# Performance work log

Measured on AMD Instinct MI355X. Metric: run time of the kernel, lower is better.

## Reference

```python
import jax, jax.numpy as jnp
import numpy as np

N = 50000
E = 800000
D = 128
L = 2
EPS = 1e-12  # BatchNorm1d eps in the module
NEG_SLOPE = 0.2  # PyG GATConv default leaky_relu slope


def setup_inputs() -> dict:
    key = jax.random.key(0)
    ks = jax.random.split(key, 12)
    x = jax.random.normal(ks[0], (N, D), dtype=jnp.float32)
    # edges guaranteed non-self (GATConv removes then re-adds self loops)
    src = jax.random.randint(ks[1], (E,), 0, N)
    off = jax.random.randint(ks[2], (E,), 1, N)
    dst = (src + off) % N
    edge_index = jnp.stack([src, dst]).astype(jnp.int64)
    scale = 1.0 / np.sqrt(D)
    Ws = jax.random.normal(ks[3], (L, D, D), dtype=jnp.float32) * scale
    a_src = jax.random.normal(ks[4], (L, D), dtype=jnp.float32) * scale
    a_dst = jax.random.normal(ks[5], (L, D), dtype=jnp.float32) * scale
    bias = jax.random.normal(ks[6], (L, D), dtype=jnp.float32) * 0.01
    gamma = jnp.ones((L, D), dtype=jnp.float32)
    beta = jnp.zeros((L, D), dtype=jnp.float32)
    run_mean = jax.random.normal(ks[7], (L, D), dtype=jnp.float32) * 0.01
    run_var = jax.random.uniform(ks[8], (L, D), minval=0.5, maxval=1.5, dtype=jnp.float32)
    return {"x": x, "edge_index": edge_index, "Ws": Ws, "a_src": a_src,
            "a_dst": a_dst, "bias": bias, "gamma": gamma, "beta": beta,
            "run_mean": run_mean, "run_var": run_var}


def _gat_layer(x, src, dst, W, asrc, adst, b):
    # x: [N, d_in]; W: [d_in, D]
    h = x @ W  # [N, D]
    e = jnp.take(h @ asrc, src) + jnp.take(h @ adst, dst)  # [E'] per-edge score
    e = jnp.where(e > 0, e, NEG_SLOPE * e)  # leaky_relu
    # segment softmax over destination node
    m = jax.ops.segment_max(e, dst, num_segments=N)
    ee = jnp.exp(e - jnp.take(m, dst))
    s = jax.ops.segment_sum(ee, dst, num_segments=N)
    alpha = ee / jnp.take(s, dst)
    # scatter-aggregate weighted source features
    msg = alpha[:, None] * jnp.take(h, src, axis=0)  # [E', D]
    out = jax.ops.segment_sum(msg, dst, num_segments=N)
    return out + b


def reference(x, edge_index, Ws, a_src, a_dst, bias, gamma, beta, run_mean, run_var):
    src, dst = edge_index[0], edge_index[1]
    # GATConv add_self_loops=True
    loops = jnp.arange(N, dtype=src.dtype)
    src = jnp.concatenate([src, loops])
    dst = jnp.concatenate([dst, loops])
    for i in range(L):
        x = _gat_layer(x, src, dst, Ws[i], a_src[i], a_dst[i], bias[i])
        # BatchNorm1d (eval mode, running stats) + ReLU
        x = (x - run_mean[i]) * (gamma[i] * jax.lax.rsqrt(run_var[i] + EPS)) + beta[i]
        x = jax.nn.relu(x)
    return x
```

## Files before the change

### kernel.cpp

```cpp
#include <hip/hip_runtime.h>

constexpr int Dd = 128;
constexpr float BN_EPS = 1e-12f;
constexpr float NEG_SLOPE = 0.2f;

using bf16x8 = __attribute__((ext_vector_type(8))) short;
using f32x4  = __attribute__((ext_vector_type(4))) float;

__device__ __forceinline__ ushort f2bf(float f) {
    unsigned u = __float_as_uint(f);
    return (ushort)((u + 0x7fffu + ((u >> 16) & 1u)) >> 16);
}

__global__ __launch_bounds__(256) void wprep_zero_kernel(
    const float* __restrict__ W, ushort* __restrict__ Wt, int* __restrict__ cntc)
{
    int t = threadIdx.x;
    if (blockIdx.x >= 2) {
        cntc[t] = 0;
        return;
    }
    __shared__ float lds[32][33];
    const float* Wl = W + (size_t)blockIdx.x * Dd * Dd;
    ushort* Wo = Wt + (size_t)blockIdx.x * Dd * Dd;
    int r = t >> 3, c4 = (t & 7) << 2;
    for (int tk = 0; tk < 4; ++tk)
    for (int tn = 0; tn < 4; ++tn) {
        int k0 = tk * 32, n0 = tn * 32;
        float4 v = *(const float4*)&Wl[(size_t)(k0 + r) * Dd + n0 + c4];
        lds[r][c4] = v.x; lds[r][c4 + 1] = v.y; lds[r][c4 + 2] = v.z; lds[r][c4 + 3] = v.w;
        __syncthreads();
        ushort4 o;
        o.x = f2bf(lds[c4 + 0][r]); o.y = f2bf(lds[c4 + 1][r]);
        o.z = f2bf(lds[c4 + 2][r]); o.w = f2bf(lds[c4 + 3][r]);
        *(ushort4*)&Wo[(size_t)(n0 + r) * Dd + k0 + c4] = o;
        __syncthreads();
    }
}

__global__ __launch_bounds__(256) void coarse_hist_kernel(
    const int* __restrict__ dst, int* __restrict__ cntc, int E, int NB)
{
    __shared__ int lh[256];
    int t = threadIdx.x;
    lh[t] = 0;
    __syncthreads();
    for (int e = blockIdx.x * 256 + t; e < E; e += gridDim.x * 256)
        atomicAdd(&lh[dst[e] >> 8], 1);
    __syncthreads();
    if (t < NB && lh[t]) atomicAdd(&cntc[t], lh[t]);
}

__global__ __launch_bounds__(256) void coarse_scan_kernel(
    const int* __restrict__ cntc, int* __restrict__ base,
    int* __restrict__ cursor, int NB, int E)
{
    __shared__ int lds[256];
    int t = threadIdx.x;
    int v0 = (t < NB) ? cntc[t] : 0;
    lds[t] = v0;
    __syncthreads();
    for (int o = 1; o < 256; o <<= 1) {
        int v = (t >= o) ? lds[t - o] : 0;
        __syncthreads();
        lds[t] += v;
        __syncthreads();
    }
    int excl = lds[t] - v0;
    if (t < NB) { base[t] = excl; cursor[t] = excl; }
    if (t == 0) base[NB] = E;
}

__global__ __launch_bounds__(256) void partition_kernel(
    const int* __restrict__ src, const int* __restrict__ dst,
    int* __restrict__ cursor, unsigned* __restrict__ gpart, int E)
{
    __shared__ int h[256], lb[256], gs[256], cur[256];
    __shared__ unsigned staged[4096];
    const int t = threadIdx.x;
    const int c0 = blockIdx.x * 4096;
    const int count = min(4096, E - c0);

    h[t] = 0; cur[t] = 0;
    __syncthreads();
#pragma unroll
    for (int j = 0; j < 16; ++j) {
        int idx = j * 256 + t;
        if (idx < count) atomicAdd(&h[dst[c0 + idx] >> 8], 1);
    }
    __syncthreads();
    {
        int v0 = h[t];
        lb[t] = v0;
        __syncthreads();
        for (int o = 1; o < 256; o <<= 1) {
            int v = (t >= o) ? lb[t - o] : 0;
            __syncthreads();
            lb[t] += v;
            __syncthreads();
        }
        lb[t] -= v0;
    }
    if (h[t]) gs[t] = atomicAdd(&cursor[t], h[t]);
    __syncthreads();
#pragma unroll
    for (int j = 0; j < 16; ++j) {
        int idx = j * 256 + t;
        if (idx < count) {
            int d = dst[c0 + idx], s = src[c0 + idx];
            int b = d >> 8;
            int pos = lb[b] + atomicAdd(&cur[b], 1);
            staged[pos] = (unsigned)s | ((unsigned)(d & 255) << 16) | ((unsigned)b << 24);
        }
    }
    __syncthreads();
#pragma unroll
    for (int j = 0; j < 16; ++j) {
        int idx = j * 256 + t;
        if (idx < count) {
            unsigned p = staged[idx];
            int b = p >> 24;
            gpart[gs[b] + (idx - lb[b])] = p;
        }
    }
}

__global__ __launch_bounds__(256) void bucket_csr_kernel(
    const unsigned* __restrict__ gpart, const int* __restrict__ base,
    int* __restrict__ rowptr, int* __restrict__ ssrc, int N, int NB, int E)
{
    __shared__ int h[256], lb[256], cur[256];
    const int t = threadIdx.x;
    const int b = blockIdx.x;
    const int cb = base[b], ce = base[b + 1];
    const int cnt = ce - cb;

    h[t] = 0; cur[t] = 0;
    __syncthreads();
    for (int o = t; o < cnt; o += 256)
        atomicAdd(&h[(gpart[cb + o] >> 16) & 255], 1);
    __syncthreads();
    {
        int v0 = h[t];
        lb[t] = v0;
        __syncthreads();
        for (int o = 1; o < 256; o <<= 1) {
            int v = (t >= o) ? lb[t - o] : 0;
            __syncthreads();
            lb[t] += v;
            __syncthreads();
        }
        lb[t] -= v0;
    }
    int n0 = b * 256 + t;
    if (n0 < N) rowptr[n0] = cb + lb[t];
    if (b == 0 && t == 0) rowptr[N] = E;
    __syncthreads();
    for (int o = t; o < cnt; o += 256) {
        unsigned p = gpart[cb + o];
        int n = (p >> 16) & 255;
        int pos = lb[n] + atomicAdd(&cur[n], 1);
        ssrc[cb + pos] = (int)(p & 0xFFFFu);
    }
}

template<bool BF16IN>
__global__ __launch_bounds__(256) void gemm_mfma(
    const void* __restrict__ Xv, const ushort* __restrict__ Wt,
    const float* __restrict__ asrc, const float* __restrict__ adst,
    ushort* __restrict__ Hb, float* __restrict__ hs, float* __restrict__ hd, int N)
{
    __shared__ ushort Xs[64 * 128];
    __shared__ ushort Bs[128 * 128];

    const int t = threadIdx.x;
    const int lane = t & 63, wid = t >> 6;
    const int row0 = blockIdx.x * 64;

    if constexpr (BF16IN) {
        const ushort* X = (const ushort*)Xv;
#pragma unroll
        for (int p = 0; p < 4; ++p) {
            int id = t + p * 256;
            int r = id >> 4, b16 = id & 15;
            int g = row0 + r;
            uint4 v = make_uint4(0, 0, 0, 0);
            if (g < N) v = *(const uint4*)&X[(size_t)g * Dd + b16 * 8];
            *(uint4*)&Xs[r * 128 + ((b16 ^ (r & 15)) << 3)] = v;
        }
    } else {
        const float* X = (const float*)Xv;
#pragma unroll
        for (int p = 0; p < 8; ++p) {
            int id = t + p * 256;
            int r = id >> 5, c4g = id & 31;
            int g = row0 + r;
            float4 v = make_float4(0.f, 0.f, 0.f, 0.f);
            if (g < N) v = *(const float4*)&X[(size_t)g * Dd + c4g * 4];
            ushort4 o; o.x = f2bf(v.x); o.y = f2bf(v.y); o.z = f2bf(v.z); o.w = f2bf(v.w);
            int b16 = c4g >> 1, sub = c4g & 1;
            *(ushort4*)&Xs[r * 128 + (((b16 ^ (r & 15)) << 3) | (sub << 2))] = o;
        }
    }
#pragma unroll
    for (int p = 0; p < 8; ++p) {
        int id = t + p * 256;
        int n = id >> 4, b16 = id & 15;
        uint4 v = *(const uint4*)&Wt[(size_t)n * 128 + b16 * 8];
        *(uint4*)&Bs[n * 128 + ((b16 ^ (n & 15)) << 3)] = v;
    }
    __syncthreads();

    f32x4 acc[8];
#pragma unroll
    for (int f = 0; f < 8; ++f) acc[f] = (f32x4){0.f, 0.f, 0.f, 0.f};

#pragma unroll
    for (int kk = 0; kk < 4; ++kk) {
        int ra = wid * 16 + (lane & 15);
        int b16 = (lane >> 4) + kk * 4;
        bf16x8 a = *(bf16x8*)&Xs[ra * 128 + ((b16 ^ (ra & 15)) << 3)];
#pragma unroll
        for (int f = 0; f < 8; ++f) {
            int nb = f * 16 + (lane & 15);
            bf16x8 b = *(bf16x8*)&Bs[nb * 128 + ((b16 ^ (nb & 15)) << 3)];
            acc[f] = __builtin_amdgcn_mfma_f32_16x16x32_bf16(a, b, acc[f], 0, 0, 0);
        }
    }

    float aS[8], aD[8];
#pragma unroll
    for (int f = 0; f < 8; ++f) {
        aS[f] = asrc[(lane & 15) + f * 16];
        aD[f] = adst[(lane & 15) + f * 16];
    }
#pragma unroll
    for (int j = 0; j < 4; ++j) {
        int r = row0 + wid * 16 + (lane >> 4) * 4 + j;
        float ps = 0.f, pd = 0.f;
#pragma unroll
        for (int f = 0; f < 8; ++f) { ps += acc[f][j] * aS[f]; pd += acc[f][j] * aD[f]; }
#pragma unroll
        for (int o = 8; o; o >>= 1) { ps += __shfl_xor(ps, o); pd += __shfl_xor(pd, o); }
        if (r < N) {
#pragma unroll
            for (int f = 0; f < 8; ++f)
                Hb[(size_t)r * Dd + (lane & 15) + f * 16] = f2bf(acc[f][j]);
            if ((lane & 15) == 0) { hs[r] = ps; hd[r] = pd; }
        }
    }
}

template<bool BF16OUT>
__global__ __launch_bounds__(256) void gat_agg_kernel(
    const int* __restrict__ rowptr, const int* __restrict__ ssrc,
    const float* __restrict__ hs, const float* __restrict__ hd,
    const ushort* __restrict__ Hb,
    const float* __restrict__ bias, const float* __restrict__ gamma,
    const float* __restrict__ beta, const float* __restrict__ mean,
    const float* __restrict__ var, void* __restrict__ outv, int N)
{
    const int wid = (blockIdx.x * 256 + threadIdx.x) >> 6;
    if (wid >= N) return;
    const int lane = threadIdx.x & 63;
    const int q = lane >> 4, li = lane & 15;
    const size_t rowO = (size_t)wid * Dd;

    const float hdi = hd[wid];
    float sc0 = hs[wid] + hdi;
    sc0 = sc0 > 0.f ? sc0 : NEG_SLOPE * sc0;
    const float w0 = (q == 0) ? __expf(sc0) : 0.f;

    float acc[8];
    float s = w0;
    {
        uint4 own = *(const uint4*)&Hb[rowO + li * 8];
#pragma unroll
        for (int k = 0; k < 4; ++k) {
            unsigned w = ((const unsigned*)&own)[k];
            acc[2 * k]     = w0 * __uint_as_float(w << 16);
            acc[2 * k + 1] = w0 * __uint_as_float(w & 0xffff0000u);
        }
    }

    const int rs = rowptr[wid];
    const int nv = rowptr[wid + 1] - rs;

    uint4 r0 = make_uint4(0, 0, 0, 0), r1 = make_uint4(0, 0, 0, 0);
    float h0 = 0.f, h1 = 0.f;
    if (q < nv) {
        int sj = ssrc[rs + q];
        h0 = hs[sj];
        r0 = *(const uint4*)&Hb[(size_t)sj * Dd + li * 8];
    }
    if (4 + q < nv) {
        int sj = ssrc[rs + 4 + q];
        h1 = hs[sj];
        r1 = *(const uint4*)&Hb[(size_t)sj * Dd + li * 8];
    }

    const int nit = (nv + 3) >> 2;
    for (int it = 0; it < nit; ++it) {
        float scv = h0 + hdi;
        scv = scv > 0.f ? scv : NEG_SLOPE * scv;
        float ee = (it * 4 + q < nv) ? __expf(scv) : 0.f;
        s += ee;
        uint4 rc = r0;
        r0 = r1; h0 = h1;
        int pn = (it + 2) * 4 + q;
        if (pn < nv) {
            int sj = ssrc[rs + pn];
            h1 = hs[sj];
            r1 = *(const uint4*)&Hb[(size_t)sj * Dd + li * 8];
        }
#pragma unroll
        for (int k = 0; k < 4; ++k) {
            unsigned w = ((const unsigned*)&rc)[k];
            acc[2 * k]     += ee * __uint_as_float(w << 16);
            acc[2 * k + 1] += ee * __uint_as_float(w & 0xffff0000u);
        }
    }

#pragma unroll
    for (int k = 0; k < 8; ++k) {
        acc[k] += __shfl_xor(acc[k], 16);
        acc[k] += __shfl_xor(acc[k], 32);
    }
    s += __shfl_xor(s, 16);
    s += __shfl_xor(s, 32);

    if (q == 0) {
        float inv = 1.0f / s;
        int c0 = li * 8;
        float o[8];
#pragma unroll
        for (int m = 0; m < 8; ++m) {
            float bm = bias[c0 + m], gm = gamma[c0 + m], btm = beta[c0 + m];
            float mnm = mean[c0 + m], vrm = var[c0 + m];
            o[m] = fmaxf((acc[m] * inv + bm - mnm) * (gm * rsqrtf(vrm + BN_EPS)) + btm, 0.f);
        }
        if constexpr (BF16OUT) {
            ushort* out = (ushort*)outv;
            uint4 pk;
#pragma unroll
            for (int k = 0; k < 4; ++k)
                ((unsigned*)&pk)[k] = (unsigned)f2bf(o[2 * k]) | ((unsigned)f2bf(o[2 * k + 1]) << 16);
            *(uint4*)&out[rowO + c0] = pk;
        } else {
            float* out = (float*)outv;
            *(float4*)&out[rowO + c0]     = make_float4(o[0], o[1], o[2], o[3]);
            *(float4*)&out[rowO + c0 + 4] = make_float4(o[4], o[5], o[6], o[7]);
        }
    }
}

extern "C" void kernel_launch(void* const* d_in, const int* in_sizes, int n_in,
                              void* d_out, int out_size, void* d_ws, size_t ws_size,
                              hipStream_t stream)
{
    const float* x     = (const float*)d_in[0];
    const int*   ei    = (const int*)d_in[1];
    const float* Ws    = (const float*)d_in[2];
    const float* a_src = (const float*)d_in[3];
    const float* a_dst = (const float*)d_in[4];
    const float* bias  = (const float*)d_in[5];
    const float* gamma = (const float*)d_in[6];
    const float* beta  = (const float*)d_in[7];
    const float* mean  = (const float*)d_in[8];
    const float* var   = (const float*)d_in[9];
    float* out = (float*)d_out;
    float* ws  = (float*)d_ws;

    const int N = in_sizes[0] / Dd;
    const int E = in_sizes[1] / 2;
    const int NB = (N + 255) >> 8;
    const int* src = ei;
    const int* dst = ei + E;

    float* hs    = ws;
    float* hd    = hs + N;
    ushort* Hb   = (ushort*)(hd + N);
    ushort* xmid = Hb + (size_t)N * Dd;
    ushort* WtB  = xmid + (size_t)N * Dd;
    int* rowptr  = (int*)(WtB + 2 * Dd * Dd);
    int* cntc    = rowptr + (N + 1);
    int* base    = cntc + 256;
    int* cursor  = base + 257;
    unsigned* gpart = (unsigned*)(cursor + 256);
    int* ssrc    = (int*)(gpart + E);

    const int gemm_blocks = (N + 63) / 64;
    const int part_blocks = (E + 4095) / 4096;
    const int agg_blocks  = (N * 64 + 255) / 256;

    wprep_zero_kernel<<<3, 256, 0, stream>>>(Ws, WtB, cntc);
    coarse_hist_kernel<<<256, 256, 0, stream>>>(dst, cntc, E, NB);
    coarse_scan_kernel<<<1, 256, 0, stream>>>(cntc, base, cursor, NB, E);
    partition_kernel<<<part_blocks, 256, 0, stream>>>(src, dst, cursor, gpart, E);
    bucket_csr_kernel<<<NB, 256, 0, stream>>>(gpart, base, rowptr, ssrc, N, NB, E);

    gemm_mfma<false><<<gemm_blocks, 256, 0, stream>>>(
        x, WtB, a_src, a_dst, Hb, hs, hd, N);
    gat_agg_kernel<true><<<agg_blocks, 256, 0, stream>>>(
        rowptr, ssrc, hs, hd, Hb, bias, gamma, beta, mean, var, (void*)xmid, N);

    gemm_mfma<true><<<gemm_blocks, 256, 0, stream>>>(
        xmid, WtB + (size_t)Dd * Dd, a_src + Dd, a_dst + Dd, Hb, hs, hd, N);
    gat_agg_kernel<false><<<agg_blocks, 256, 0, stream>>>(
        rowptr, ssrc, hs, hd, Hb, bias + Dd, gamma + Dd, beta + Dd,
        mean + Dd, var + Dd, (void*)out, N);
}
```

Measured before the change: 253.3 us.

## Aggregate GAT messages with MFMA over 16-node groups using precomputed fp16 edge weights

Replaces the per-node wave gather-accumulate with a separate edge-weight kernel and an MFMA-based aggregation. The edge-weight kernel computes a max-stabilized softmax numerator per edge, stored as fp16 tagged with the local node id. The aggregation kernel stages 32 gathered source rows per chunk in LDS, reads them back with transposed loads, and multiplies them by a masked 16x32 weight matrix on fp16 MFMA. A ones-vector MFMA produces the softmax denominators. Self loops are now folded into the CSR, H is stored as fp16 instead of bf16, and the BatchNorm affine is precomputed into scale and shift vectors. The aim is to move the weighted sum onto matrix cores, at the cost of an extra kernel pass, wasted MFMA lanes on sparse rows, and reduced fp16 range.

Result: slower. 345.3 us (+36.3%).

```diff
diff --git a/kernel.cpp b/kernel.cpp
--- a/kernel.cpp
+++ b/kernel.cpp
@@ -5,19 +5,27 @@
 constexpr float NEG_SLOPE = 0.2f;
 
 using bf16x8 = __attribute__((ext_vector_type(8))) short;
+using f16x8  = __attribute__((ext_vector_type(8))) _Float16;
 using f32x4  = __attribute__((ext_vector_type(4))) float;
 
 __device__ __forceinline__ ushort f2bf(float f) {
     unsigned u = __float_as_uint(f);
     return (ushort)((u + 0x7fffu + ((u >> 16) & 1u)) >> 16);
 }
+__device__ __forceinline__ float lrelu(float x) { return x > 0.f ? x : NEG_SLOPE * x; }
 
 __global__ __launch_bounds__(256) void wprep_zero_kernel(
-    const float* __restrict__ W, ushort* __restrict__ Wt, int* __restrict__ cntc)
+    const float* __restrict__ W, ushort* __restrict__ Wt, int* __restrict__ cntc,
+    const float* __restrict__ bias, const float* __restrict__ gamma,
+    const float* __restrict__ beta, const float* __restrict__ mean,
+    const float* __restrict__ var, float* __restrict__ kA, float* __restrict__ kB)
 {
     int t = threadIdx.x;
     if (blockIdx.x >= 2) {
         cntc[t] = 0;
+        float sc = gamma[t] * rsqrtf(var[t] + BN_EPS);
+        kA[t] = sc;
+        kB[t] = (bias[t] - mean[t]) * sc + beta[t];
         return;
     }
     __shared__ float lds[32][33];
@@ -127,12 +135,13 @@
 
 __global__ __launch_bounds__(256) void bucket_csr_kernel(
     const unsigned* __restrict__ gpart, const int* __restrict__ base,
-    int* __restrict__ rowptr, int* __restrict__ ssrc, int N, int NB, int E)
+    int* __restrict__ rowptr, int* __restrict__ ssrc, int N, int NB, int Etot)
 {
     __shared__ int h[256], lb[256], cur[256];
     const int t = threadIdx.x;
     const int b = blockIdx.x;
     const int cb = base[b], ce = base[b + 1];
+    const int cb2 = cb + b * 256;
     const int cnt = ce - cb;
 
     h[t] = 0; cur[t] = 0;
@@ -153,14 +162,18 @@
         lb[t] -= v0;
     }
     int n0 = b * 256 + t;
-    if (n0 < N) rowptr[n0] = cb + lb[t];
-    if (b == 0 && t == 0) rowptr[N] = E;
+    if (n0 < N) {
+        int rp = cb2 + lb[t] + t;
+        rowptr[n0] = rp;
+        ssrc[rp] = n0;
+    }
+    if (b == 0 && t == 0) rowptr[N] = Etot;
     __syncthreads();
     for (int o = t; o < cnt; o += 256) {
         unsigned p = gpart[cb + o];
         int n = (p >> 16) & 255;
         int pos = lb[n] + atomicAdd(&cur[n], 1);
-        ssrc[cb + pos] = (int)(p & 0xFFFFu);
+        ssrc[cb2 + pos + n + 1] = (int)(p & 0xFFFFu);
     }
 }
 
@@ -168,7 +181,7 @@
 __global__ __launch_bounds__(256) void gemm_mfma(
     const void* __restrict__ Xv, const ushort* __restrict__ Wt,
     const float* __restrict__ asrc, const float* __restrict__ adst,
-    ushort* __restrict__ Hb, float* __restrict__ hs, float* __restrict__ hd, int N)
+    _Float16* __restrict__ Hf, float* __restrict__ hs, float* __restrict__ hd, int N)
 {
     __shared__ ushort Xs[64 * 128];
     __shared__ ushort Bs[128 * 128];
@@ -245,111 +258,154 @@
         if (r < N) {
 #pragma unroll
             for (int f = 0; f < 8; ++f)
-                Hb[(size_t)r * Dd + (lane & 15) + f * 16] = f2bf(acc[f][j]);
+                Hf[(size_t)r * Dd + (lane & 15) + f * 16] = (_Float16)acc[f][j];
             if ((lane & 15) == 0) { hs[r] = ps; hd[r] = pd; }
         }
     }
 }
 
-template<bool BF16OUT>
-__global__ __launch_bounds__(256) void gat_agg_kernel(
+__global__ __launch_bounds__(256) void edge_weight_kernel(
     const int* __restrict__ rowptr, const int* __restrict__ ssrc,
     const float* __restrict__ hs, const float* __restrict__ hd,
-    const ushort* __restrict__ Hb,
-    const float* __restrict__ bias, const float* __restrict__ gamma,
-    const float* __restrict__ beta, const float* __restrict__ mean,
-    const float* __restrict__ var, void* __restrict__ outv, int N)
-{
-    const int wid = (blockIdx.x * 256 + threadIdx.x) >> 6;
-    if (wid >= N) return;
-    const int lane = threadIdx.x & 63;
-    const int q = lane >> 4, li = lane & 15;
-    const size_t rowO = (size_t)wid * Dd;
-
-    const float hdi = hd[wid];
-    float sc0 = hs[wid] + hdi;
-    sc0 = sc0 > 0.f ? sc0 : NEG_SLOPE * sc0;
-    const float w0 = (q == 0) ? __expf(sc0) : 0.f;
-
-    float acc[8];
-    float s = w0;
+    unsigned* __restrict__ ew, int N)
+{
+    int t = threadIdx.x;
+    int wid = (blockIdx.x * 256 + t) >> 6;
+    int lane = t & 63, q = lane >> 4, c = lane & 15;
+    int n = wid * 4 + q;
+    if (n >= N) return;
+    int rs = rowptr[n], re = rowptr[n + 1];
+    float mx = -1e30f;
+    for (int p = rs + c; p < re; p += 16) mx = fmaxf(mx, hs[ssrc[p]]);
+#pragma unroll
+    for (int o = 1; o < 16; o <<= 1) mx = fmaxf(mx, __shfl_xor(mx, o));
+    float hdn = hd[n];
+    float M = lrelu(mx + hdn);
+    unsigned nid = (unsigned)(n & 15) << 16;
+    for (int p = rs + c; p < re; p += 16) {
+        float sc = lrelu(hs[ssrc[p]] + hdn);
+        float e = __expf(sc - M);
+        ew[p] = nid | (unsigned)__builtin_bit_cast(unsigned short, (_Float16)e);
+    }
+}
+
+#define TRRD(dst, addr, off) \
+    asm volatile("ds_read_b64_tr_b16 %0, %1 offset:" #off : "=v"(dst) : "v"(addr))
+
+template<bool BF16OUT>
+__global__ __launch_bounds__(256) void gat_mfma_agg(
+    const int* __restrict__ rowptr, const int* __restrict__ ssrc,
+    const unsigned* __restrict__ ew, const _Float16* __restrict__ Hf,
+    const float* __restrict__ kA, const float* __restrict__ kB,
+    void* __restrict__ outv, int N, int NG)
+{
+    __shared__ _Float16 stage[4][4096];
+    const int t = threadIdx.x;
+    const int wv = t >> 6, lane = t & 63;
+    const int g = blockIdx.x * 4 + wv;
+    if (g >= NG) return;
+    const int q = lane >> 4, c = lane & 15;
+
+    const int gs = rowptr[g * 16];
+    const int ge = rowptr[min(g * 16 + 16, N)];
+    const int gl = ge - 1;
+
+    const int sk = lane >> 1, sh = lane & 1;
+    uint4* wb = (uint4*)&stage[wv][0];
+    const int wi_base = (sk >> 2) * 64 + sh * 32 + (sk & 3) * 2;
+    const uint4* __restrict__ Hf4 = (const uint4*)Hf;
+
+    const unsigned ldsbase = (unsigned)(uintptr_t)(void*)&stage[wv][0];
+    const unsigned rb = ldsbase + q * 2048 + 8 * c;
+
+    f32x4 acc[8];
+#pragma unroll
+    for (int f = 0; f < 8; ++f) acc[f] = (f32x4){0.f, 0.f, 0.f, 0.f};
+    f32x4 accs = (f32x4){0.f, 0.f, 0.f, 0.f};
+
+    union { unsigned u[4]; f16x8 h; } ONES;
+#pragma unroll
+    for (int p = 0; p < 4; ++p) ONES.u[p] = 0x3C003C00u;
+
+    const int nch = (ge - gs + 31) >> 5;
+    uint4 hvA[8], hvB[8];
+
     {
-        uint4 own = *(const uint4*)&Hb[rowO + li * 8];
-#pragma unroll
-        for (int k = 0; k < 4; ++k) {
-            unsigned w = ((const unsigned*)&own)[k];
-            acc[2 * k]     = w0 * __uint_as_float(w << 16);
-            acc[2 * k + 1] = w0 * __uint_as_float(w & 0xffff0000u);
-        }
-    }
-
-    const int rs = rowptr[wid];
-    const int nv = rowptr[wid + 1] - rs;
-
-    uint4 r0 = make_uint4(0, 0, 0, 0), r1 = make_uint4(0, 0, 0, 0);
-    float h0 = 0.f, h1 = 0.f;
-    if (q < nv) {
-        int sj = ssrc[rs + q];
-        h0 = hs[sj];
-        r0 = *(const uint4*)&Hb[(size_t)sj * Dd + li * 8];
-    }
-    if (4 + q < nv) {
-        int sj = ssrc[rs + 4 + q];
-        h1 = hs[sj];
-        r1 = *(const uint4*)&Hb[(size_t)sj * Dd + li * 8];
-    }
-
-    const int nit = (nv + 3) >> 2;
-    for (int it = 0; it < nit; ++it) {
-        float scv = h0 + hdi;
-        scv = scv > 0.f ? scv : NEG_SLOPE * scv;
-        float ee = (it * 4 + q < nv) ? __expf(scv) : 0.f;
-        s += ee;
-        uint4 rc = r0;
-        r0 = r1; h0 = h1;
-        int pn = (it + 2) * 4 + q;
-        if (pn < nv) {
-            int sj = ssrc[rs + pn];
-            h1 = hs[sj];
-            r1 = *(const uint4*)&Hb[(size_t)sj * Dd + li * 8];
-        }
-#pragma unroll
-        for (int k = 0; k < 4; ++k) {
-            unsigned w = ((const unsigned*)&rc)[k];
-            acc[2 * k]     += ee * __uint_as_float(w << 16);
-            acc[2 * k + 1] += ee * __uint_as_float(w & 0xffff0000u);
-        }
-    }
-
-#pragma unroll
-    for (int k = 0; k < 8; ++k) {
-        acc[k] += __shfl_xor(acc[k], 16);
-        acc[k] += __shfl_xor(acc[k], 32);
-    }
-    s += __shfl_xor(s, 16);
-    s += __shfl_xor(s, 32);
-
-    if (q == 0) {
-        float inv = 1.0f / s;
-        int c0 = li * 8;
-        float o[8];
-#pragma unroll
-        for (int m = 0; m < 8; ++m) {
-            float bm = bias[c0 + m], gm = gamma[c0 + m], btm = beta[c0 + m];
-            float mnm = mean[c0 + m], vrm = var[c0 + m];
-            o[m] = fmaxf((acc[m] * inv + bm - mnm) * (gm * rsqrtf(vrm + BN_EPS)) + btm, 0.f);
-        }
-        if constexpr (BF16OUT) {
-            ushort* out = (ushort*)outv;
-            uint4 pk;
-#pragma unroll
-            for (int k = 0; k < 4; ++k)
-                ((unsigned*)&pk)[k] = (unsigned)f2bf(o[2 * k]) | ((unsigned)f2bf(o[2 * k + 1]) << 16);
-            *(uint4*)&out[rowO + c0] = pk;
-        } else {
-            float* out = (float*)outv;
-            *(float4*)&out[rowO + c0]     = make_float4(o[0], o[1], o[2], o[3]);
-            *(float4*)&out[rowO + c0 + 4] = make_float4(o[4], o[5], o[6], o[7]);
+        int srck = ssrc[min(gs + sk, gl)];
+        const uint4* hr = &Hf4[(size_t)srck * 16 + sh * 8];
+#pragma unroll
+        for (int i = 0; i < 8; ++i) hvA[i] = hr[i];
+    }
+
+#define AGG_BODY(HV_CUR, HV_NXT, CH)                                                    \
+    {                                                                                   \
+        const int cb = gs + (CH) * 32;                                                  \
+        const int abase = cb + q * 8;                                                   \
+        unsigned aw[8];                                                                 \
+        _Pragma("unroll")                                                               \
+        for (int e = 0; e < 8; ++e) aw[e] = ew[min(abase + e, gl)];                     \
+        union { unsigned u[4]; f16x8 h; } A;                                            \
+        _Pragma("unroll")                                                               \
+        for (int p = 0; p < 4; ++p) {                                                   \
+            unsigned lo = (abase + 2 * p     < ge && (aw[2 * p]     >> 16) == (unsigned)c) ? (aw[2 * p]     & 0xFFFFu) : 0u; \
+            unsigned hi = (abase + 2 * p + 1 < ge && (aw[2 * p + 1] >> 16) == (unsigned)c) ? (aw[2 * p + 1] & 0xFFFFu) : 0u; \
+            A.u[p] = lo | (hi << 16);                                                   \
+        }                                                                               \
+        _Pragma("unroll")                                                               \
+        for (int i = 0; i < 8; ++i)                                                     \
+            wb[wi_base + (i >> 1) * 8 + (i & 1)] = HV_CUR[i];                           \
+                   \
+        {                                                                               \
+            int srcn = ssrc[min(cb + 32 + sk, gl)];                                     \
+            const uint4* hrn = &Hf4[(size_t)srcn * 16 + sh * 8];                        \
+            _Pragma("unroll")                                                           \
+            for (int i = 0; i < 8; ++i) HV_NXT[i] = hrn[i];                             \
+        }                                                                               \
+        asm volatile("s_waitcnt lgkmcnt(0)" ::: "memory");                              \
+        uint2 blo[8], bhi[8];                                                           \
+        TRRD(blo[0], rb, 0);    TRRD(bhi[0], rb, 1024);                                 \
+        TRRD(blo[1], rb, 128);  TRRD(bhi[1], rb, 1152);                                 \
+        TRRD(blo[2], rb, 256);  TRRD(bhi[2], rb, 1280);                                 \
+        TRRD(blo[3], rb, 384);  TRRD(bhi[3], rb, 1408);                                 \
+        TRRD(blo[4], rb, 512);  TRRD(bhi[4], rb, 1536);                                 \
+        TRRD(blo[5], rb, 640);  TRRD(bhi[5], rb, 1664);                                 \
+        TRRD(blo[6], rb, 768);  TRRD(bhi[6], rb, 1792);                                 \
+        TRRD(blo[7], rb, 896);  TRRD(bhi[7], rb, 1920);                                 \
+        asm volatile("s_waitcnt lgkmcnt(0)" ::: "memory");                              \
+        __builtin_amdgcn_sched_barrier(0);                                              \
+        _Pragma("unroll")                                                               \
+        for (int nb = 0; nb < 8; ++nb) {                                                \
+            union { unsigned u[4]; f16x8 h; } B;                                        \
+            B.u[0] = blo[nb].x; B.u[1] = blo[nb].y;                                     \
+            B.u[2] = bhi[nb].x; B.u[3] = bhi[nb].y;                                     \
+            acc[nb] = __builtin_amdgcn_mfma_f32_16x16x32_f16(A.h, B.h, acc[nb], 0, 0, 0); \
+        }                                                                               \
+        accs = __builtin_amdgcn_mfma_f32_16x16x32_f16(A.h, ONES.h, accs, 0, 0, 0);      \
+    }
+
+    int ch = 0;
+    while (ch < nch) {
+        AGG_BODY(hvA, hvB, ch); ++ch;
+        if (ch >= nch) break;
+        AGG_BODY(hvB, hvA, ch); ++ch;
+    }
+#undef AGG_BODY
+
+    float ka[8], kb[8];
+#pragma unroll
+    for (int nb = 0; nb < 8; ++nb) { ka[nb] = kA[nb * 16 + c]; kb[nb] = kB[nb * 16 + c]; }
+#pragma unroll
+    for (int j = 0; j < 4; ++j) {
+        int node = g * 16 + q * 4 + j;
+        if (node >= N) continue;
+        float inv = 1.0f / accs[j];
+#pragma unroll
+        for (int nb = 0; nb < 8; ++nb) {
+            float o = fmaxf(acc[nb][j] * inv * ka[nb] + kb[nb], 0.f);
+            if constexpr (BF16OUT)
+                ((ushort*)outv)[(size_t)node * Dd + nb * 16 + c] = f2bf(o);
+            else
+                ((float*)outv)[(size_t)node * Dd + nb * 16 + c] = o;
         }
     }
 }
@@ -373,40 +429,56 @@
 
     const int N = in_sizes[0] / Dd;
     const int E = in_sizes[1] / 2;
+    const int Etot = E + N;
     const int NB = (N + 255) >> 8;
+    const int NG = (N + 15) >> 4;
     const int* src = ei;
     const int* dst = ei + E;
 
-    float* hs    = ws;
-    float* hd    = hs + N;
-    ushort* Hb   = (ushort*)(hd + N);
-    ushort* xmid = Hb + (size_t)N * Dd;
-    ushort* WtB  = xmid + (size_t)N * Dd;
-    int* rowptr  = (int*)(WtB + 2 * Dd * Dd);
+    float*    hs   = ws;
+    float*    hd   = hs + N;
+    _Float16* Hf   = (_Float16*)(hd + N);
+    ushort*   xmid = (ushort*)(Hf + (size_t)N * Dd);
+    ushort*   WtB  = xmid + (size_t)N * Dd;
+    float*    kAB  = (float*)(WtB + 2 * Dd * Dd);
+    int* rowptr  = (int*)(kAB + 512);
     int* cntc    = rowptr + (N + 1);
     int* base    = cntc + 256;
     int* cursor  = base + 257;
     unsigned* gpart = (unsigned*)(cursor + 256);
     int* ssrc    = (int*)(gpart + E);
+    unsigned* ew = (unsigned*)(ssrc + Etot);
 
     const int gemm_blocks = (N + 63) / 64;
     const int part_blocks = (E + 4095) / 4096;
-    const int agg_blocks  = (N * 64 + 255) / 256;
-
-    wprep_zero_kernel<<<3, 256, 0, stream>>>(Ws, WtB, cntc);
+    const int ew_blocks   = (N * 16 + 255) / 256;
+    const int agg_blocks  = (NG + 3) / 4;
+
+    wprep_zero_kernel<<<3, 256, 0, stream>>>(Ws, WtB, cntc, bias, gamma, beta, mean, var,
+                                             kAB, kAB + 256);
     coarse_hist_kernel<<<256, 256, 0, stream>>>(dst, cntc, E, NB);
     coarse_scan_kernel<<<1, 256, 0, stream>>>(cntc, base, cursor, NB, E);
     partition_kernel<<<part_blocks, 256, 0, stream>>>(src, dst, cursor, gpart, E);
-    bucket_csr_kernel<<<NB, 256, 0, stream>>>(gpart, base, rowptr, ssrc, N, NB, E);
-
-    gemm_mfma<false><<<gemm_blocks, 256, 0, stream>>>(
-        x, WtB, a_src, a_dst, Hb, hs, hd, N);
-    gat_agg_kernel<true><<<agg_blocks, 256, 0, stream>>>(
-        rowptr, ssrc, hs, hd, Hb, bias, gamma, beta, mean, var, (void*)xmid, N);
-
-    gemm_mfma<true><<<gemm_blocks, 256, 0, stream>>>(
-        xmid, WtB + (size_t)Dd * Dd, a_src + Dd, a_dst + Dd, Hb, hs, hd, N);
-    gat_agg_kernel<false><<<agg_blocks, 256, 0, stream>>>(
-        rowptr, ssrc, hs, hd, Hb, bias + Dd, gamma + Dd, beta + Dd,
-        mean + Dd, var + Dd, (void*)out, N);
-}
+    bucket_csr_kernel<<<NB, 256, 0, stream>>>(gpart, base, rowptr, ssrc, N, NB, Etot);
+
+    for (int l = 0; l < 2; ++l) {
+        const float* kA_l = kAB + l * 128;
+        const float* kB_l = kAB + 256 + l * 128;
+
+        if (l == 0)
+            gemm_mfma<false><<<gemm_blocks, 256, 0, stream>>>(
+                (const void*)x, WtB, a_src, a_dst, Hf, hs, hd, N);
+        else
+            gemm_mfma<true><<<gemm_blocks, 256, 0, stream>>>(
+                (const void*)xmid, WtB + (size_t)Dd * Dd, a_src + Dd, a_dst + Dd, Hf, hs, hd, N);
+
+        edge_weight_kernel<<<ew_blocks, 256, 0, stream>>>(rowptr, ssrc, hs, hd, ew, N);
+
+        if (l == 0)
+            gat_mfma_agg<true><<<agg_blocks, 256, 0, stream>>>(
+                rowptr, ssrc, ew, Hf, kA_l, kB_l, (void*)xmid, N, NG);
+        else
+            gat_mfma_agg<false><<<agg_blocks, 256, 0, stream>>>(
+                rowptr, ssrc, ew, Hf, kA_l, kB_l, (void*)out, N, NG);
+    }
+}
```

## Fold self-loops into CSR, store H as fp16, precompute BN affine

Applied to the files above, without the earlier changes.

Self-loop edges are now placed directly into the CSR by the bucket kernel, which shifts each row's offset so it holds its own node first. This removes the separate own-row load and exp from the aggregation prologue. The intermediate H is stored as fp16 instead of bf16, and the aggregation converts it with a plain cast and FMA. Bias and BatchNorm are folded into per-channel scale and shift vectors in the prep kernel, so the epilogue loads two float4 pairs instead of five scalars per channel. The bucket kernel's ssrc writes become scattered, and fp16 risks overflow if activations grow large.

Result: faster. 242.7 us (-4.2%).

```diff
diff --git a/kernel.cpp b/kernel.cpp
--- a/kernel.cpp
+++ b/kernel.cpp
@@ -11,13 +11,20 @@
     unsigned u = __float_as_uint(f);
     return (ushort)((u + 0x7fffu + ((u >> 16) & 1u)) >> 16);
 }
+__device__ __forceinline__ float lrelu(float x) { return x > 0.f ? x : NEG_SLOPE * x; }
 
 __global__ __launch_bounds__(256) void wprep_zero_kernel(
-    const float* __restrict__ W, ushort* __restrict__ Wt, int* __restrict__ cntc)
+    const float* __restrict__ W, ushort* __restrict__ Wt, int* __restrict__ cntc,
+    const float* __restrict__ bias, const float* __restrict__ gamma,
+    const float* __restrict__ beta, const float* __restrict__ mean,
+    const float* __restrict__ var, float* __restrict__ kA, float* __restrict__ kB)
 {
     int t = threadIdx.x;
     if (blockIdx.x >= 2) {
         cntc[t] = 0;
+        float sc = gamma[t] * rsqrtf(var[t] + BN_EPS);
+        kA[t] = sc;
+        kB[t] = (bias[t] - mean[t]) * sc + beta[t];
         return;
     }
     __shared__ float lds[32][33];
@@ -127,12 +134,13 @@
 
 __global__ __launch_bounds__(256) void bucket_csr_kernel(
     const unsigned* __restrict__ gpart, const int* __restrict__ base,
-    int* __restrict__ rowptr, int* __restrict__ ssrc, int N, int NB, int E)
+    int* __restrict__ rowptr, int* __restrict__ ssrc, int N, int NB, int Etot)
 {
     __shared__ int h[256], lb[256], cur[256];
     const int t = threadIdx.x;
     const int b = blockIdx.x;
     const int cb = base[b], ce = base[b + 1];
+    const int cb2 = cb + b * 256;
     const int cnt = ce - cb;
 
     h[t] = 0; cur[t] = 0;
@@ -153,14 +161,18 @@
         lb[t] -= v0;
     }
     int n0 = b * 256 + t;
-    if (n0 < N) rowptr[n0] = cb + lb[t];
-    if (b == 0 && t == 0) rowptr[N] = E;
+    if (n0 < N) {
+        int rp = cb2 + lb[t] + t;
+        rowptr[n0] = rp;
+        ssrc[rp] = n0;
+    }
+    if (b == 0 && t == 0) rowptr[N] = Etot;
     __syncthreads();
     for (int o = t; o < cnt; o += 256) {
         unsigned p = gpart[cb + o];
         int n = (p >> 16) & 255;
         int pos = lb[n] + atomicAdd(&cur[n], 1);
-        ssrc[cb + pos] = (int)(p & 0xFFFFu);
+        ssrc[cb2 + pos + n + 1] = (int)(p & 0xFFFFu);
     }
 }
 
@@ -168,7 +180,7 @@
 __global__ __launch_bounds__(256) void gemm_mfma(
     const void* __restrict__ Xv, const ushort* __restrict__ Wt,
     const float* __restrict__ asrc, const float* __restrict__ adst,
-    ushort* __restrict__ Hb, float* __restrict__ hs, float* __restrict__ hd, int N)
+    _Float16* __restrict__ Hf, float* __restrict__ hs, float* __restrict__ hd, int N)
 {
     __shared__ ushort Xs[64 * 128];
     __shared__ ushort Bs[128 * 128];
@@ -245,7 +257,7 @@
         if (r < N) {
 #pragma unroll
             for (int f = 0; f < 8; ++f)
-                Hb[(size_t)r * Dd + (lane & 15) + f * 16] = f2bf(acc[f][j]);
+                Hf[(size_t)r * Dd + (lane & 15) + f * 16] = (_Float16)acc[f][j];
             if ((lane & 15) == 0) { hs[r] = ps; hd[r] = pd; }
         }
     }
@@ -255,10 +267,9 @@
 __global__ __launch_bounds__(256) void gat_agg_kernel(
     const int* __restrict__ rowptr, const int* __restrict__ ssrc,
     const float* __restrict__ hs, const float* __restrict__ hd,
-    const ushort* __restrict__ Hb,
-    const float* __restrict__ bias, const float* __restrict__ gamma,
-    const float* __restrict__ beta, const float* __restrict__ mean,
-    const float* __restrict__ var, void* __restrict__ outv, int N)
+    const _Float16* __restrict__ Hf,
+    const float* __restrict__ kA, const float* __restrict__ kB,
+    void* __restrict__ outv, int N)
 {
     const int wid = (blockIdx.x * 256 + threadIdx.x) >> 6;
     if (wid >= N) return;
@@ -267,36 +278,26 @@
     const size_t rowO = (size_t)wid * Dd;
 
     const float hdi = hd[wid];
-    float sc0 = hs[wid] + hdi;
-    sc0 = sc0 > 0.f ? sc0 : NEG_SLOPE * sc0;
-    const float w0 = (q == 0) ? __expf(sc0) : 0.f;
-
     float acc[8];
-    float s = w0;
-    {
-        uint4 own = *(const uint4*)&Hb[rowO + li * 8];
-#pragma unroll
-        for (int k = 0; k < 4; ++k) {
-            unsigned w = ((const unsigned*)&own)[k];
-            acc[2 * k]     = w0 * __uint_as_float(w << 16);
-            acc[2 * k + 1] = w0 * __uint_as_float(w & 0xffff0000u);
-        }
-    }
+#pragma unroll
+    for (int m = 0; m < 8; ++m) acc[m] = 0.f;
+    float s = 0.f;
 
     const int rs = rowptr[wid];
     const int nv = rowptr[wid + 1] - rs;
 
-    uint4 r0 = make_uint4(0, 0, 0, 0), r1 = make_uint4(0, 0, 0, 0);
+    union HU { uint4 u; _Float16 h[8]; };
+    HU r0, r1; r0.u = make_uint4(0,0,0,0); r1.u = make_uint4(0,0,0,0);
     float h0 = 0.f, h1 = 0.f;
     if (q < nv) {
         int sj = ssrc[rs + q];
         h0 = hs[sj];
-        r0 = *(const uint4*)&Hb[(size_t)sj * Dd + li * 8];
+        r0.u = *(const uint4*)&Hf[(size_t)sj * Dd + li * 8];
     }
     if (4 + q < nv) {
         int sj = ssrc[rs + 4 + q];
         h1 = hs[sj];
-        r1 = *(const uint4*)&Hb[(size_t)sj * Dd + li * 8];
+        r1.u = *(const uint4*)&Hf[(size_t)sj * Dd + li * 8];
     }
 
     const int nit = (nv + 3) >> 2;
@@ -305,26 +306,23 @@
         scv = scv > 0.f ? scv : NEG_SLOPE * scv;
         float ee = (it * 4 + q < nv) ? __expf(scv) : 0.f;
         s += ee;
-        uint4 rc = r0;
+        HU rc = r0;
         r0 = r1; h0 = h1;
         int pn = (it + 2) * 4 + q;
         if (pn < nv) {
             int sj = ssrc[rs + pn];
             h1 = hs[sj];
-            r1 = *(const uint4*)&Hb[(size_t)sj * Dd + li * 8];
-        }
-#pragma unroll
-        for (int k = 0; k < 4; ++k) {
-            unsigned w = ((const unsigned*)&rc)[k];
-            acc[2 * k]     += ee * __uint_as_float(w << 16);
-            acc[2 * k + 1] += ee * __uint_as_float(w & 0xffff0000u);
-        }
-    }
-
-#pragma unroll
-    for (int k = 0; k < 8; ++k) {
-        acc[k] += __shfl_xor(acc[k], 16);
-        acc[k] += __shfl_xor(acc[k], 32);
+            r1.u = *(const uint4*)&Hf[(size_t)sj * Dd + li * 8];
+        }
+#pragma unroll
+        for (int m = 0; m < 8; ++m)
+            acc[m] = fmaf((float)rc.h[m], ee, acc[m]);
+    }
+
+#pragma unroll
+    for (int m = 0; m < 8; ++m) {
+        acc[m] += __shfl_xor(acc[m], 16);
+        acc[m] += __shfl_xor(acc[m], 32);
     }
     s += __shfl_xor(s, 16);
     s += __shfl_xor(s, 32);
@@ -332,13 +330,17 @@
     if (q == 0) {
         float inv = 1.0f / s;
         int c0 = li * 8;
+        float4 ka0 = *(const float4*)&kA[c0],     ka1 = *(const float4*)&kA[c0 + 4];
+        float4 kb0 = *(const float4*)&kB[c0],     kb1 = *(const float4*)&kB[c0 + 4];
         float o[8];
-#pragma unroll
-        for (int m = 0; m < 8; ++m) {
-            float bm = bias[c0 + m], gm = gamma[c0 + m], btm = beta[c0 + m];
-            float mnm = mean[c0 + m], vrm = var[c0 + m];
-            o[m] = fmaxf((acc[m] * inv + bm - mnm) * (gm * rsqrtf(vrm + BN_EPS)) + btm, 0.f);
-        }
+        o[0] = fmaxf(acc[0] * inv * ka0.x + kb0.x, 0.f);
+        o[1] = fmaxf(acc[1] * inv * ka0.y + kb0.y, 0.f);
+        o[2] = fmaxf(acc[2] * inv * ka0.z + kb0.z, 0.f);
+        o[3] = fmaxf(acc[3] * inv * ka0.w + kb0.w, 0.f);
+        o[4] = fmaxf(acc[4] * inv * ka1.x + kb1.x, 0.f);
+        o[5] = fmaxf(acc[5] * inv * ka1.y + kb1.y, 0.f);
+        o[6] = fmaxf(acc[6] * inv * ka1.z + kb1.z, 0.f);
+        o[7] = fmaxf(acc[7] * inv * ka1.w + kb1.w, 0.f);
         if constexpr (BF16OUT) {
             ushort* out = (ushort*)outv;
             uint4 pk;
@@ -373,16 +375,18 @@
 
     const int N = in_sizes[0] / Dd;
     const int E = in_sizes[1] / 2;
+    const int Etot = E + N;
     const int NB = (N + 255) >> 8;
     const int* src = ei;
     const int* dst = ei + E;
 
-    float* hs    = ws;
-    float* hd    = hs + N;
-    ushort* Hb   = (ushort*)(hd + N);
-    ushort* xmid = Hb + (size_t)N * Dd;
-    ushort* WtB  = xmid + (size_t)N * Dd;
-    int* rowptr  = (int*)(WtB + 2 * Dd * Dd);
+    float*    hs   = ws;
+    float*    hd   = hs + N;
+    _Float16* Hf   = (_Float16*)(hd + N);
+    ushort*   xmid = (ushort*)(Hf + (size_t)N * Dd);
+    ushort*   WtB  = xmid + (size_t)N * Dd;
+    float*    kAB  = (float*)(WtB + 2 * Dd * Dd);
+    int* rowptr  = (int*)(kAB + 512);
     int* cntc    = rowptr + (N + 1);
     int* base    = cntc + 256;
     int* cursor  = base + 257;
@@ -393,20 +397,29 @@
     const int part_blocks = (E + 4095) / 4096;
     const int agg_blocks  = (N * 64 + 255) / 256;
 
-    wprep_zero_kernel<<<3, 256, 0, stream>>>(Ws, WtB, cntc);
+    wprep_zero_kernel<<<3, 256, 0, stream>>>(Ws, WtB, cntc, bias, gamma, beta, mean, var,
+                                             kAB, kAB + 256);
     coarse_hist_kernel<<<256, 256, 0, stream>>>(dst, cntc, E, NB);
     coarse_scan_kernel<<<1, 256, 0, stream>>>(cntc, base, cursor, NB, E);
     partition_kernel<<<part_blocks, 256, 0, stream>>>(src, dst, cursor, gpart, E);
-    bucket_csr_kernel<<<NB, 256, 0, stream>>>(gpart, base, rowptr, ssrc, N, NB, E);
-
-    gemm_mfma<false><<<gemm_blocks, 256, 0, stream>>>(
-        x, WtB, a_src, a_dst, Hb, hs, hd, N);
-    gat_agg_kernel<true><<<agg_blocks, 256, 0, stream>>>(
-        rowptr, ssrc, hs, hd, Hb, bias, gamma, beta, mean, var, (void*)xmid, N);
-
-    gemm_mfma<true><<<gemm_blocks, 256, 0, stream>>>(
-        xmid, WtB + (size_t)Dd * Dd, a_src + Dd, a_dst + Dd, Hb, hs, hd, N);
-    gat_agg_kernel<false><<<agg_blocks, 256, 0, stream>>>(
-        rowptr, ssrc, hs, hd, Hb, bias + Dd, gamma + Dd, beta + Dd,
-        mean + Dd, var + Dd, (void*)out, N);
-}
+    bucket_csr_kernel<<<NB, 256, 0, stream>>>(gpart, base, rowptr, ssrc, N, NB, Etot);
+
+    for (int l = 0; l < 2; ++l) {
+        const float* kA_l = kAB + l * 128;
+        const float* kB_l = kAB + 256 + l * 128;
+
+        if (l == 0)
+            gemm_mfma<false><<<gemm_blocks, 256, 0, stream>>>(
+                (const void*)x, WtB, a_src, a_dst, Hf, hs, hd, N);
+        else
+            gemm_mfma<true><<<gemm_blocks, 256, 0, stream>>>(
+                (const void*)xmid, WtB + (size_t)Dd * Dd, a_src + Dd, a_dst + Dd, Hf, hs, hd, N);
+
+        if (l == 0)
+            gat_agg_kernel<true><<<agg_blocks, 256, 0, stream>>>(
+                rowptr, ssrc, hs, hd, Hf, kA_l, kB_l, (void*)xmid, N);
+        else
+            gat_agg_kernel<false><<<agg_blocks, 256, 0, stream>>>(
+                rowptr, ssrc, hs, hd, Hf, kA_l, kB_l, (void*)out, N);
+    }
+}
```
